# Kernel tuning notes

Hardware: AMD Instinct MI355X
Metric: run time of the kernel (lower is better)

Reference implementation:

```python
import jax, jax.numpy as jnp
import numpy as np

OUT, IN, GS = 11008, 4096, 128   # out_features, in_features, group_size
G = IN // GS                     # num_groups = 32 (in_features divisible by group_size)
TOKENS = 8192                    # batch 4 * seq 2048


def setup_inputs() -> dict:
    key = jax.random.key(0)
    k1, k2, k3, k4, k5 = jax.random.split(key, 5)
    x = jax.random.normal(k1, (TOKENS, IN), dtype=jnp.float32)
    # packed int4 weights: two nibbles per byte, stored as int32 in [0,256)
    qweight = jax.random.randint(k2, (OUT, IN // 2), 0, 256, dtype=jnp.int32)
    # realistic GPTQ scales (small positive) and zero-points in [0,15]
    scales = jax.random.uniform(k3, (OUT, G), dtype=jnp.float32) * 0.01 + 1e-3
    zeros = jax.random.uniform(k4, (OUT, G), dtype=jnp.float32) * 15.0
    bias = jax.random.normal(k5, (OUT,), dtype=jnp.float32) * 0.01
    return {"x": x, "qweight": qweight, "scales": scales, "zeros": zeros, "bias": bias}


def _dequant(qweight, scales, zeros):
    # unpack: column 2i = low nibble, column 2i+1 = high nibble (matches torch loop)
    low = (qweight & 15).astype(jnp.float32)          # [OUT, IN/2]
    high = ((qweight >> 4) & 15).astype(jnp.float32)  # [OUT, IN/2]
    w = jnp.stack([low, high], axis=-1).reshape(OUT, IN)
    # group-wise dequant: (q - zero) * scale per group of GS input channels
    w = (w.reshape(OUT, G, GS) - zeros[:, :, None]) * scales[:, :, None]
    return w.reshape(OUT, IN)


def reference(x, qweight, scales, zeros, bias):
    w = _dequant(qweight, scales, zeros)   # [OUT, IN] fp32
    # F.linear: x @ w.T + bias
    return jnp.einsum('ti,oi->to', x, w) + bias
```

## Files before the change

kernel.cpp:

```cpp
#include <hip/hip_runtime.h>
#include <stdint.h>

#define OUTF 11008
#define INF  4096
#define NG   32
#define TOK  8192
#define KB4  2048

#define BM 256
#define BN 256
#define BK 64
#define NT (INF / BK)
#define GX (OUTF / BN)
#define GY (TOK / BM)
#define NWG (GX * GY)

typedef unsigned short u16;
typedef __attribute__((ext_vector_type(8))) short bf16x8;
typedef __attribute__((ext_vector_type(4))) float f32x4;

__device__ inline u16 f2bf(float f) {
  union { float f; uint32_t u; } v; v.f = f;
  return (u16)((v.u + 0x7fff + ((v.u >> 16) & 1)) >> 16);
}

__device__ inline void async_copy16(const void* g, const void* l) {
  __builtin_amdgcn_global_load_lds(
      (__attribute__((address_space(1))) void*)(g),
      (__attribute__((address_space(3))) void*)(l), 16, 0, 0);
}

#define FENCE() asm volatile("" ::: "memory")
#define BAR()   do { FENCE(); __builtin_amdgcn_s_barrier(); FENCE(); } while (0)
#define VMCNT(n) asm volatile("s_waitcnt vmcnt(" #n ")" ::: "memory")


#define NXU ((long long)TOK * INF / 4)
#define NWU ((long long)OUTF * KB4 / 4)
#define PREPBLK 2048

__global__ __launch_bounds__(256) void prep(const float* __restrict__ X,
                                            const int* __restrict__ QW,
                                            const float* __restrict__ scales,
                                            const float* __restrict__ zeros,
                                            u16* __restrict__ Xb,
                                            u16* __restrict__ Wb) {
  const long long stride = (long long)gridDim.x * 256;
  for (long long i = (long long)blockIdx.x * 256 + threadIdx.x; i < NXU + NWU;
       i += stride) {
    if (i < NXU) {
      const float4 f = ((const float4*)X)[i];
      union { u16 t[4]; uint2 v; } u;
      u.t[0] = f2bf(f.x); u.t[1] = f2bf(f.y);
      u.t[2] = f2bf(f.z); u.t[3] = f2bf(f.w);
      ((uint2*)Xb)[i] = u.v;
    } else {
      const long long j = i - NXU;
      const int o = (int)(j >> 9);
      const int c0 = ((int)j & 511) * 4;
      const int g = c0 >> 6;
      const float s = scales[o * NG + g];
      const float zs = -zeros[o * NG + g] * s;
      const int4 q = ((const int4*)QW)[j];
      const int qq[4] = {q.x, q.y, q.z, q.w};
      union { u16 t[8]; int4 v; } u;
#pragma unroll
      for (int k = 0; k < 4; ++k) {
        u.t[2 * k]     = f2bf(fmaf((float)(qq[k] & 15), s, zs));
        u.t[2 * k + 1] = f2bf(fmaf((float)((qq[k] >> 4) & 15), s, zs));
      }
      ((int4*)Wb)[j] = u.v;
    }
  }
}


__global__ __launch_bounds__(512, 2) void gemm_pre512(const u16* __restrict__ A,
                                                      const u16* __restrict__ B,
                                                      const float* __restrict__ bias,
                                                      float* __restrict__ C) {
  __shared__ __align__(16) u16 As[2][BM * BK];
  __shared__ __align__(16) u16 Bs[2][BN * BK];
  const int tid = threadIdx.x;
  const int lane = tid & 63;
  const int wid = __builtin_amdgcn_readfirstlane(tid >> 6);

  const int lin = blockIdx.x;
  const int wg = (lin & 7) * (NWG / 8) + (lin >> 3);
  const int bm = wg / GX;
  const int bn = wg % GX;

  const u16* Ab = A + (size_t)bm * BM * INF;
  const u16* Bb = B + (size_t)bn * BN * INF;

  const int rowoff = tid >> 3;
  const int gran = (tid & 7) ^ (rowoff & 7);
  const u16* Asrc = Ab + (size_t)rowoff * INF + gran * 8;
  const u16* Bsrc = Bb + (size_t)rowoff * INF + gran * 8;
  const int wid8 = wid * 8;

  const int rr = lane & 15;
  const int q4 = lane >> 4;
  const int wm = wid >> 2;
  const int wn = wid & 3;

  f32x4 acc[8][4] = {};
  bf16x8 af[4];
  bf16x8 bfv[4];

#define STAGE1(LDS, SRC, TT, R0)                                               \
  async_copy16((SRC) + (size_t)(R0) * INF + (size_t)(TT) * BK,                 \
               (const char*)(LDS) + ((R0) + wid8) * 128);

#define STAGE_ALL(S, TT)                                                       \
  do {                                                                         \
    STAGE1(&As[S][0], Asrc, TT, 0)   STAGE1(&As[S][0], Asrc, TT, 64)           \
    STAGE1(&As[S][0], Asrc, TT, 128) STAGE1(&As[S][0], Asrc, TT, 192)          \
    STAGE1(&Bs[S][0], Bsrc, TT, 0)   STAGE1(&Bs[S][0], Bsrc, TT, 64)           \
    STAGE1(&Bs[S][0], Bsrc, TT, 128) STAGE1(&Bs[S][0], Bsrc, TT, 192)          \
  } while (0)

#define PH_READ_A(S, KS, MH)                                                   \
  _Pragma("unroll") for (int mi = 0; mi < 4; ++mi)                             \
    af[mi] = *(const bf16x8*)&As[S][(wm * 128 + ((MH) * 4 + mi) * 16 + rr) *   \
                                        BK +                                   \
                                    ((((KS) * 4 + q4) ^ (rr & 7)) * 8)];

#define PH_READ_B(S, KS)                                                       \
  _Pragma("unroll") for (int ni = 0; ni < 4; ++ni)                             \
    bfv[ni] = *(const bf16x8*)&Bs[S][(wn * 64 + ni * 16 + rr) * BK +           \
                                     ((((KS) * 4 + q4) ^ (rr & 7)) * 8)];

#define PH_MFMA(MH)                                                            \
  do {                                                                         \
    __builtin_amdgcn_s_setprio(1);                                             \
    _Pragma("unroll") for (int mi = 0; mi < 4; ++mi)                           \
      _Pragma("unroll") for (int ni = 0; ni < 4; ++ni)                         \
        acc[(MH) * 4 + mi][ni] = __builtin_amdgcn_mfma_f32_16x16x32_bf16(      \
            af[mi], bfv[ni], acc[(MH) * 4 + mi][ni], 0, 0, 0);                 \
    __builtin_amdgcn_s_setprio(0);                                             \
  } while (0)

#define TILE(S, T)                                                             \
  do {                                                                         \
    PH_READ_A(S, 0, 0); PH_READ_B(S, 0); PH_MFMA(0);                           \
    PH_READ_A(S, 0, 1); PH_MFMA(1);                                            \
    PH_READ_A(S, 1, 0); PH_READ_B(S, 1); PH_MFMA(0);                           \
    PH_READ_A(S, 1, 1); PH_MFMA(1);                                            \
    BAR();                                  \
    if ((T) + 2 < NT) { STAGE_ALL(S, (T) + 2); VMCNT(8); } else { VMCNT(0); }  \
    BAR();                         \
  } while (0)

  STAGE_ALL(0, 0);
  STAGE_ALL(1, 1);
  VMCNT(8);
  BAR();

  for (int t = 0; t < NT; t += 2) {
    TILE(0, t);
    TILE(1, t + 1);
  }

  const int ncol = lane & 15;
  const int qrow = (lane >> 4) * 4;
  float bv[4];
#pragma unroll
  for (int ni = 0; ni < 4; ++ni)
    bv[ni] = bias[bn * BN + wn * 64 + ni * 16 + ncol];
#pragma unroll
  for (int mi = 0; mi < 8; ++mi)
#pragma unroll
    for (int ni = 0; ni < 4; ++ni) {
      const int gn = bn * BN + wn * 64 + ni * 16 + ncol;
#pragma unroll
      for (int r = 0; r < 4; ++r) {
        const int gm = bm * BM + wm * 128 + mi * 16 + qrow + r;
        C[(size_t)gm * OUTF + gn] = acc[mi][ni][r] + bv[ni];
      }
    }
}


#define FBM 128
#define FBN 128

#define FMFMA_COMPUTE()                                                       \
  do {                                                                        \
    const int frr = lane & 15;                                                \
    const int fq4 = lane >> 4;                                                \
    _Pragma("unroll") for (int ks = 0; ks < 2; ++ks) {                        \
      bf16x8 fa[4], fb[4];                                                    \
      const int kk = (((ks * 4 + fq4) ^ (frr & 7)) * 8);                      \
      _Pragma("unroll") for (int i = 0; i < 4; ++i) {                         \
        fa[i] = *(const bf16x8*)&Asf[(mwave + i * 16 + frr) * BK + kk];       \
        fb[i] = *(const bf16x8*)&Bsf[(nwave + i * 16 + frr) * BK + kk];       \
      }                                                                       \
      _Pragma("unroll") for (int mi = 0; mi < 4; ++mi)                        \
        _Pragma("unroll") for (int ni = 0; ni < 4; ++ni)                      \
          facc[mi][ni] = __builtin_amdgcn_mfma_f32_16x16x32_bf16(             \
              fa[mi], fb[ni], facc[mi][ni], 0, 0, 0);                         \
    }                                                                         \
  } while (0)

__global__ __launch_bounds__(256) void gemm_fused(const float* __restrict__ X,
                                                  const int* __restrict__ QW,
                                                  const float* __restrict__ scales,
                                                  const float* __restrict__ zeros,
                                                  const float* __restrict__ bias,
                                                  float* __restrict__ C) {
  __shared__ __align__(16) u16 Asf[FBM * BK];
  __shared__ __align__(16) u16 Bsf[FBN * BK];
  const int tid = threadIdx.x;
  const int lane = tid & 63;
  const int wid = tid >> 6;
  const int bm = blockIdx.y, bn = blockIdx.x;
  const int row = tid >> 1;
  const int half = tid & 1;
  const float* xr = X + (size_t)(bm * FBM + row) * INF + half * 32;
  const int* qr = QW + (size_t)(bn * FBN + row) * KB4 + half * 16;
  const float* srow = scales + (size_t)(bn * FBN + row) * NG;
  const float* zrow = zeros + (size_t)(bn * FBN + row) * NG;
  const int mwave = (wid >> 1) * 64;
  const int nwave = (wid & 1) * 64;
  f32x4 facc[4][4] = {};

  for (int kb = 0; kb < INF / BK; ++kb) {
    const int k0 = kb * BK;
    union { u16 t[32]; int4 v[4]; } ta, tb;
#pragma unroll
    for (int j = 0; j < 8; ++j) {
      const float4 f = *(const float4*)(xr + k0 + j * 4);
      ta.t[4 * j]     = f2bf(f.x);
      ta.t[4 * j + 1] = f2bf(f.y);
      ta.t[4 * j + 2] = f2bf(f.z);
      ta.t[4 * j + 3] = f2bf(f.w);
    }
    {
      const float s = srow[kb >> 1];
      const float zs = -zrow[kb >> 1] * s;
#pragma unroll
      for (int j = 0; j < 4; ++j) {
        const int4 q = *(const int4*)(qr + kb * 32 + j * 4);
        const int qq[4] = {q.x, q.y, q.z, q.w};
#pragma unroll
        for (int u = 0; u < 4; ++u) {
          tb.t[8 * j + 2 * u]     = f2bf(fmaf((float)(qq[u] & 15), s, zs));
          tb.t[8 * j + 2 * u + 1] = f2bf(fmaf((float)((qq[u] >> 4) & 15), s, zs));
        }
      }
    }
    __syncthreads();
#pragma unroll
    for (int j = 0; j < 4; ++j) {
      *(int4*)&Asf[row * BK + (((half * 4 + j) ^ (row & 7)) * 8)] = ta.v[j];
      *(int4*)&Bsf[row * BK + (((half * 4 + j) ^ (row & 7)) * 8)] = tb.v[j];
    }
    __syncthreads();
    FMFMA_COMPUTE();
  }
  {
    const int ncol = lane & 15;
    const int qrow = (lane >> 4) * 4;
#pragma unroll
    for (int mi = 0; mi < 4; ++mi)
#pragma unroll
      for (int ni = 0; ni < 4; ++ni) {
        const int gn = bn * FBN + nwave + ni * 16 + ncol;
        const float bvv = bias[gn];
#pragma unroll
        for (int r = 0; r < 4; ++r) {
          const int gm = bm * FBM + mwave + mi * 16 + qrow + r;
          C[(size_t)gm * OUTF + gn] = facc[mi][ni][r] + bvv;
        }
      }
  }
}


extern "C" void kernel_launch(void* const* d_in, const int* in_sizes, int n_in,
                              void* d_out, int out_size, void* d_ws, size_t ws_size,
                              hipStream_t stream) {
  const float* x = (const float*)d_in[0];
  const int* qw = (const int*)d_in[1];
  const float* scales = (const float*)d_in[2];
  const float* zeros = (const float*)d_in[3];
  const float* bias = (const float*)d_in[4];
  float* out = (float*)d_out;

  const size_t needW = (size_t)OUTF * INF * sizeof(u16);
  const size_t needX = (size_t)TOK * INF * sizeof(u16);

  if (ws_size >= needW + needX) {
    u16* Wb = (u16*)d_ws;
    u16* Xb = (u16*)((char*)d_ws + needW);
    prep<<<PREPBLK, 256, 0, stream>>>(x, qw, scales, zeros, Xb, Wb);
    gemm_pre512<<<dim3(NWG), 512, 0, stream>>>(Xb, Wb, bias, out);
  } else {
    gemm_fused<<<dim3(OUTF / FBN, TOK / FBM), 256, 0, stream>>>(x, qw, scales, zeros, bias, out);
  }
}
```

Measured before the change: 1.275 ms.

## Double-buffer MFMA register fragments and merge the two tile barriers into one

```diff
diff --git a/kernel.cpp b/kernel.cpp
--- a/kernel.cpp
+++ b/kernel.cpp
@@ -33,6 +33,7 @@
 #define FENCE() asm volatile("" ::: "memory")
 #define BAR()   do { FENCE(); __builtin_amdgcn_s_barrier(); FENCE(); } while (0)
 #define VMCNT(n) asm volatile("s_waitcnt vmcnt(" #n ")" ::: "memory")
+#define LGKM0()  asm volatile("s_waitcnt lgkmcnt(0)" ::: "memory")
 
 
 #define NXU ((long long)TOK * INF / 4)
@@ -105,8 +106,8 @@
   const int wn = wid & 3;
 
   f32x4 acc[8][4] = {};
-  bf16x8 af[4];
-  bf16x8 bfv[4];
+  bf16x8 aLo[4][2], aHi[4][2];
+  bf16x8 bP[2][2], bQ[2][2];
 
 #define STAGE1(LDS, SRC, TT, R0)                                               \
   async_copy16((SRC) + (size_t)(R0) * INF + (size_t)(TT) * BK,                 \
@@ -120,46 +121,57 @@
     STAGE1(&Bs[S][0], Bsrc, TT, 128) STAGE1(&Bs[S][0], Bsrc, TT, 192)          \
   } while (0)
 
-#define PH_READ_A(S, KS, MH)                                                   \
+#define RD_A(DST, S, MH)                                                       \
   _Pragma("unroll") for (int mi = 0; mi < 4; ++mi)                             \
-    af[mi] = *(const bf16x8*)&As[S][(wm * 128 + ((MH) * 4 + mi) * 16 + rr) *   \
-                                        BK +                                   \
-                                    ((((KS) * 4 + q4) ^ (rr & 7)) * 8)];
-
-#define PH_READ_B(S, KS)                                                       \
-  _Pragma("unroll") for (int ni = 0; ni < 4; ++ni)                             \
-    bfv[ni] = *(const bf16x8*)&Bs[S][(wn * 64 + ni * 16 + rr) * BK +           \
-                                     ((((KS) * 4 + q4) ^ (rr & 7)) * 8)];
-
-#define PH_MFMA(MH)                                                            \
+    _Pragma("unroll") for (int ks = 0; ks < 2; ++ks)                           \
+      DST[mi][ks] = *(const bf16x8*)&As[S][                                    \
+          (wm * 128 + (MH) * 64 + mi * 16 + rr) * BK +                         \
+          (((ks * 4 + q4) ^ (rr & 7)) * 8)];
+
+#define RD_B(DST, S, NH)                                                       \
+  _Pragma("unroll") for (int ni = 0; ni < 2; ++ni)                             \
+    _Pragma("unroll") for (int ks = 0; ks < 2; ++ks)                           \
+      DST[ni][ks] = *(const bf16x8*)&Bs[S][                                    \
+          (wn * 64 + (NH) * 32 + ni * 16 + rr) * BK +                         \
+          (((ks * 4 + q4) ^ (rr & 7)) * 8)];
+
+#define MFMAQ(AQ, BQm, MH, NH)                                                 \
   do {                                                                         \
     __builtin_amdgcn_s_setprio(1);                                             \
-    _Pragma("unroll") for (int mi = 0; mi < 4; ++mi)                           \
-      _Pragma("unroll") for (int ni = 0; ni < 4; ++ni)                         \
-        acc[(MH) * 4 + mi][ni] = __builtin_amdgcn_mfma_f32_16x16x32_bf16(      \
-            af[mi], bfv[ni], acc[(MH) * 4 + mi][ni], 0, 0, 0);                 \
+    _Pragma("unroll") for (int ks = 0; ks < 2; ++ks)                           \
+      _Pragma("unroll") for (int mi = 0; mi < 4; ++mi)                         \
+        _Pragma("unroll") for (int ni = 0; ni < 2; ++ni)                       \
+          acc[(MH) * 4 + mi][(NH) * 2 + ni] =                                  \
+              __builtin_amdgcn_mfma_f32_16x16x32_bf16(                         \
+                  AQ[mi][ks], BQm[ni][ks],                                     \
+                  acc[(MH) * 4 + mi][(NH) * 2 + ni], 0, 0, 0);                 \
     __builtin_amdgcn_s_setprio(0);                                             \
   } while (0)
 
-#define TILE(S, T)                                                             \
+#define TILE(S, T, BX, BYv)                                                    \
   do {                                                                         \
-    PH_READ_A(S, 0, 0); PH_READ_B(S, 0); PH_MFMA(0);                           \
-    PH_READ_A(S, 0, 1); PH_MFMA(1);                                            \
-    PH_READ_A(S, 1, 0); PH_READ_B(S, 1); PH_MFMA(0);                           \
-    PH_READ_A(S, 1, 1); PH_MFMA(1);                                            \
-    BAR();                                  \
-    if ((T) + 2 < NT) { STAGE_ALL(S, (T) + 2); VMCNT(8); } else { VMCNT(0); }  \
-    BAR();                         \
+    RD_B(BYv, S, 1);                         \
+    MFMAQ(aLo, BX, 0, 0);                                                      \
+    RD_A(aHi, S, 1);                         \
+    MFMAQ(aLo, BYv, 0, 1);                                                     \
+    LGKM0(); VMCNT(0); BAR();          \
+    if ((T) + 2 < NT) STAGE_ALL(S, (T) + 2);                                   \
+    if ((T) + 1 < NT) RD_A(aLo, (S) ^ 1, 0);      \
+    MFMAQ(aHi, BYv, 1, 1);                                                     \
+    if ((T) + 1 < NT) RD_B(BYv, (S) ^ 1, 0);      \
+    MFMAQ(aHi, BX, 1, 0);                                                      \
   } while (0)
 
   STAGE_ALL(0, 0);
   STAGE_ALL(1, 1);
   VMCNT(8);
   BAR();
+  RD_A(aLo, 0, 0);
+  RD_B(bP, 0, 0);
 
   for (int t = 0; t < NT; t += 2) {
-    TILE(0, t);
-    TILE(1, t + 1);
+    TILE(0, t, bP, bQ);
+    TILE(1, t + 1, bQ, bP);
   }
 
   const int ncol = lane & 15;
```

Measured after the change: 1.265 ms. Within noise of the previous version (-0.8%).

## Interleave global-to-LDS staging with per-phase MFMA blocks in main loop

Applied to the files above, without the earlier changes.

```diff
diff --git a/kernel.cpp b/kernel.cpp
--- a/kernel.cpp
+++ b/kernel.cpp
@@ -105,61 +105,107 @@
   const int wn = wid & 3;
 
   f32x4 acc[8][4] = {};
-  bf16x8 af[4];
-  bf16x8 bfv[4];
+  bf16x8 bq[4];
 
 #define STAGE1(LDS, SRC, TT, R0)                                               \
   async_copy16((SRC) + (size_t)(R0) * INF + (size_t)(TT) * BK,                 \
                (const char*)(LDS) + ((R0) + wid8) * 128);
 
-#define STAGE_ALL(S, TT)                                                       \
-  do {                                                                         \
-    STAGE1(&As[S][0], Asrc, TT, 0)   STAGE1(&As[S][0], Asrc, TT, 64)           \
-    STAGE1(&As[S][0], Asrc, TT, 128) STAGE1(&As[S][0], Asrc, TT, 192)          \
-    STAGE1(&Bs[S][0], Bsrc, TT, 0)   STAGE1(&Bs[S][0], Bsrc, TT, 64)           \
-    STAGE1(&Bs[S][0], Bsrc, TT, 128) STAGE1(&Bs[S][0], Bsrc, TT, 192)          \
-  } while (0)
-
-#define PH_READ_A(S, KS, MH)                                                   \
+#define RD_A4(DST, S, KS, MH)                                                  \
   _Pragma("unroll") for (int mi = 0; mi < 4; ++mi)                             \
-    af[mi] = *(const bf16x8*)&As[S][(wm * 128 + ((MH) * 4 + mi) * 16 + rr) *   \
-                                        BK +                                   \
-                                    ((((KS) * 4 + q4) ^ (rr & 7)) * 8)];
-
-#define PH_READ_B(S, KS)                                                       \
+    DST[mi] = *(const bf16x8*)&As[S][                                          \
+        (wm * 128 + (MH) * 64 + mi * 16 + rr) * BK +                           \
+        ((((KS) * 4 + q4) ^ (rr & 7)) * 8)];
+
+#define RD_B4(DST, S, KS)                                                      \
   _Pragma("unroll") for (int ni = 0; ni < 4; ++ni)                             \
-    bfv[ni] = *(const bf16x8*)&Bs[S][(wn * 64 + ni * 16 + rr) * BK +           \
-                                     ((((KS) * 4 + q4) ^ (rr & 7)) * 8)];
-
-#define PH_MFMA(MH)                                                            \
+    DST[ni] = *(const bf16x8*)&Bs[S][                                          \
+        (wn * 64 + ni * 16 + rr) * BK +                                        \
+        ((((KS) * 4 + q4) ^ (rr & 7)) * 8)];
+
+#define MFMA16(RA, RB, MH)                                                     \
   do {                                                                         \
     __builtin_amdgcn_s_setprio(1);                                             \
     _Pragma("unroll") for (int mi = 0; mi < 4; ++mi)                           \
       _Pragma("unroll") for (int ni = 0; ni < 4; ++ni)                         \
         acc[(MH) * 4 + mi][ni] = __builtin_amdgcn_mfma_f32_16x16x32_bf16(      \
-            af[mi], bfv[ni], acc[(MH) * 4 + mi][ni], 0, 0, 0);                 \
+            RA[mi], RB[ni], acc[(MH) * 4 + mi][ni], 0, 0, 0);                  \
     __builtin_amdgcn_s_setprio(0);                                             \
   } while (0)
 
-#define TILE(S, T)                                                             \
-  do {                                                                         \
-    PH_READ_A(S, 0, 0); PH_READ_B(S, 0); PH_MFMA(0);                           \
-    PH_READ_A(S, 0, 1); PH_MFMA(1);                                            \
-    PH_READ_A(S, 1, 0); PH_READ_B(S, 1); PH_MFMA(0);                           \
-    PH_READ_A(S, 1, 1); PH_MFMA(1);                                            \
-    BAR();                                  \
-    if ((T) + 2 < NT) { STAGE_ALL(S, (T) + 2); VMCNT(8); } else { VMCNT(0); }  \
-    BAR();                         \
-  } while (0)
-
-  STAGE_ALL(0, 0);
-  STAGE_ALL(1, 1);
-  VMCNT(8);
+  STAGE1(&As[0][0], Asrc, 0, 0)   STAGE1(&As[0][0], Asrc, 0, 128)
+  STAGE1(&As[0][0], Asrc, 0, 64)  STAGE1(&As[0][0], Asrc, 0, 192)
+  STAGE1(&Bs[0][0], Bsrc, 0, 0)   STAGE1(&Bs[0][0], Bsrc, 0, 64)
+  STAGE1(&Bs[0][0], Bsrc, 0, 128) STAGE1(&Bs[0][0], Bsrc, 0, 192)
+  STAGE1(&As[1][0], Asrc, 1, 0)   STAGE1(&As[1][0], Asrc, 1, 128)
+  VMCNT(2);
   BAR();
 
   for (int t = 0; t < NT; t += 2) {
-    TILE(0, t);
-    TILE(1, t + 1);
+    {
+      bf16x8 ra[4];
+      RD_A4(ra, 0, 0, 0) RD_B4(bq, 0, 0)
+      STAGE1(&Bs[1][0], Bsrc, t + 1, 0) STAGE1(&Bs[1][0], Bsrc, t + 1, 64)
+      BAR(); MFMA16(ra, bq, 0); BAR();
+    }
+    {
+      bf16x8 ra[4];
+      RD_A4(ra, 0, 0, 1)
+      STAGE1(&Bs[1][0], Bsrc, t + 1, 128) STAGE1(&Bs[1][0], Bsrc, t + 1, 192)
+      BAR(); MFMA16(ra, bq, 1); BAR();
+    }
+    {
+      bf16x8 ra[4];
+      RD_A4(ra, 0, 1, 0) RD_B4(bq, 0, 1)
+      STAGE1(&As[1][0], Asrc, t + 1, 64) STAGE1(&As[1][0], Asrc, t + 1, 192)
+      BAR(); MFMA16(ra, bq, 0); BAR();
+    }
+    {
+      bf16x8 ra[4];
+      RD_A4(ra, 0, 1, 1)
+      if (t + 2 < NT) {
+        STAGE1(&As[0][0], Asrc, t + 2, 0) STAGE1(&As[0][0], Asrc, t + 2, 128)
+        VMCNT(2);
+      } else {
+        VMCNT(0);
+      }
+      BAR(); MFMA16(ra, bq, 1); BAR();
+    }
+    {
+      bf16x8 ra[4];
+      RD_A4(ra, 1, 0, 0) RD_B4(bq, 1, 0)
+      if (t + 2 < NT) {
+        STAGE1(&Bs[0][0], Bsrc, t + 2, 0) STAGE1(&Bs[0][0], Bsrc, t + 2, 64)
+      }
+      BAR(); MFMA16(ra, bq, 0); BAR();
+    }
+    {
+      bf16x8 ra[4];
+      RD_A4(ra, 1, 0, 1)
+      if (t + 2 < NT) {
+        STAGE1(&Bs[0][0], Bsrc, t + 2, 128) STAGE1(&Bs[0][0], Bsrc, t + 2, 192)
+      }
+      BAR(); MFMA16(ra, bq, 1); BAR();
+    }
+    {
+      bf16x8 ra[4];
+      RD_A4(ra, 1, 1, 0) RD_B4(bq, 1, 1)
+      if (t + 2 < NT) {
+        STAGE1(&As[0][0], Asrc, t + 2, 64) STAGE1(&As[0][0], Asrc, t + 2, 192)
+      }
+      BAR(); MFMA16(ra, bq, 0); BAR();
+    }
+    {
+      bf16x8 ra[4];
+      RD_A4(ra, 1, 1, 1)
+      if (t + 3 < NT) {
+        STAGE1(&As[1][0], Asrc, t + 3, 0) STAGE1(&As[1][0], Asrc, t + 3, 128)
+        VMCNT(2);
+      } else {
+        VMCNT(0);
+      }
+      BAR(); MFMA16(ra, bq, 1); BAR();
+    }
   }
 
   const int ncol = lane & 15;
```

After: 1.296 ms. About the same (+1.6%).
